# Kernel tuning notes

Hardware: AMD Instinct MI355X
Metric: run time of the kernel (lower is better)

The kernel has to match this reference:

```python
import jax, jax.numpy as jnp
import numpy as np

D_MODEL = 1024
NUM_HEAD = 16


def setup_inputs() -> dict:
    key = jax.random.key(0)
    ks = jax.random.split(key, 11)
    B, S, D = 2, 2048, D_MODEL
    scale = 1.0 / np.sqrt(D)
    inp = {
        "Q": jax.random.normal(ks[0], (B, S, D), jnp.float32),
        "K": jax.random.normal(ks[1], (B, S, D), jnp.float32),
        "V": jax.random.normal(ks[2], (B, S, D), jnp.float32),
        "Wq": jax.random.normal(ks[3], (D, D), jnp.float32) * scale,
        "bq": jax.random.normal(ks[4], (D,), jnp.float32) * 0.01,
        "Wk": jax.random.normal(ks[5], (D, D), jnp.float32) * scale,
        "bk": jax.random.normal(ks[6], (D,), jnp.float32) * 0.01,
        "Wv": jax.random.normal(ks[7], (D, D), jnp.float32) * scale,
        "bv": jax.random.normal(ks[8], (D,), jnp.float32) * 0.01,
        "Wo": jax.random.normal(ks[9], (D, D), jnp.float32) * scale,
        "bo": jax.random.normal(ks[10], (D,), jnp.float32) * 0.01,
    }
    return inp


def reference(Q, K, V, Wq, bq, Wk, bk, Wv, bv, Wo, bo):
    b, vc, d_model = Q.shape
    h = NUM_HEAD
    hd = d_model // h
    # projections (torch Linear: x @ W.T + b)
    q = (Q @ Wq.T + bq).reshape(b, vc, h, hd)
    k = (K @ Wk.T + bk).reshape(b, vc, h, hd)
    v = (V @ Wv.T + bv).reshape(b, vc, h, hd)
    # scores [b,h,q,k]
    atten = jnp.einsum('bqhd,bkhd->bhqk', q, k) / np.sqrt(hd).astype(jnp.float32)
    atten = jax.nn.softmax(atten, axis=3)
    # weighted values -> [b,q,h,hd]
    out = jnp.einsum('bhqd,bdhv->bqhv', atten, v).reshape(b, vc, d_model)
    return out @ Wo.T + bo
```

## Files before the change

### kernel.cpp

```cpp
#include <hip/hip_runtime.h>

#define S_LEN 2048
#define DM 1024
#define NH 16
#define HD 64
#define NB 2

typedef unsigned short u16;
typedef __attribute__((ext_vector_type(8))) short s16x8;
typedef __attribute__((ext_vector_type(8))) unsigned short u16x8;
typedef __attribute__((ext_vector_type(4))) float fx4;
typedef __attribute__((ext_vector_type(2))) unsigned u32x2;

__device__ __forceinline__ u16 f2bf(float f) {
  unsigned u = __builtin_bit_cast(unsigned, f);
  return (u16)((u + 0x7FFFu + ((u >> 16) & 1u)) >> 16);
}

__device__ __forceinline__ unsigned cvt_pk_bf16(float a, float b) {
  unsigned r;
  asm("v_cvt_pk_bf16_f32 %0, %1, %2" : "=v"(r) : "v"(a), "v"(b));
  return r;
}

__device__ __forceinline__ void gload16(const void* g, void* l) {
  __builtin_amdgcn_global_load_lds(
      (const __attribute__((address_space(1))) unsigned*)g,
      (__attribute__((address_space(3))) unsigned*)l, 16, 0, 0);
}

__device__ __forceinline__ fx4 mfma16(s16x8 a, s16x8 b, fx4 c) {
  return __builtin_amdgcn_mfma_f32_16x16x32_bf16(a, b, c, 0, 0, 0);
}

__global__ __launch_bounds__(256) void cvt_all_kernel(
    const float* __restrict__ Q, const float* __restrict__ K,
    const float* __restrict__ V, const float* __restrict__ Wq,
    const float* __restrict__ Wk, const float* __restrict__ Wv,
    const float* __restrict__ Wo, u16* __restrict__ Qc, u16* __restrict__ Kc,
    u16* __restrict__ Vc, u16* __restrict__ Wqb, u16* __restrict__ Wkb,
    u16* __restrict__ Wvb, u16* __restrict__ Wob) {
  const int blk = blockIdx.x;
  const float* src;
  u16* dst;
  float scale = 1.0f;
  int off;
  if (blk < 2048)      { src = Q;  dst = Qc;  off = blk; }
  else if (blk < 4096) { src = K;  dst = Kc;  off = blk - 2048; }
  else if (blk < 6144) { src = V;  dst = Vc;  off = blk - 4096; }
  else if (blk < 6656) { src = Wq; dst = Wqb; off = blk - 6144; scale = 0.18033688f; }
  else if (blk < 7168) { src = Wk; dst = Wkb; off = blk - 6656; }
  else if (blk < 7680) { src = Wv; dst = Wvb; off = blk - 7168; }
  else                 { src = Wo; dst = Wob; off = blk - 7680; }
  const int i = (off * 256 + (int)threadIdx.x) * 8;
  fx4 a = *(const fx4*)(src + i);
  fx4 b = *(const fx4*)(src + i + 4);
  u16x8 o;
  o[0] = f2bf(a[0] * scale); o[1] = f2bf(a[1] * scale);
  o[2] = f2bf(a[2] * scale); o[3] = f2bf(a[3] * scale);
  o[4] = f2bf(b[0] * scale); o[5] = f2bf(b[1] * scale);
  o[6] = f2bf(b[2] * scale); o[7] = f2bf(b[3] * scale);
  *(u16x8*)(dst + i) = o;
}

__device__ __forceinline__ void store_out(u16* C, size_t idx, float v) { C[idx] = f2bf(v); }
__device__ __forceinline__ void store_out(float* C, size_t idx, float v) { C[idx] = v; }

template <typename OUT>
__device__ __forceinline__ void gemm_pipe_body(const u16* __restrict__ A,
                                               const u16* __restrict__ Bt,
                                               const float* __restrict__ bias,
                                               float bscale, OUT* __restrict__ C,
                                               u16* __restrict__ vt, bool vout,
                                               int m0, int n0) {
  __shared__ u16 Al[3][128 * 32];
  __shared__ u16 Bl[3][128 * 32];
  const int tid = threadIdx.x;
  const int wid = tid >> 6, lane = tid & 63;
  const int g = lane >> 4, lr = lane & 15;
  const int wr = wid >> 1, wc = wid & 1;
  const int row0 = tid >> 2, ch = tid & 3;
  const int chx = ch ^ ((row0 >> 1) & 3);

  fx4 acc[4][4] = {};

  auto stage = [&](u16* Ab, u16* Bb, int k0) {
    gload16(A + (size_t)(m0 + row0) * 1024 + k0 + chx * 8, (char*)Ab + wid * 1024);
    gload16(A + (size_t)(m0 + 64 + row0) * 1024 + k0 + chx * 8,
            (char*)Ab + 4096 + wid * 1024);
    gload16(Bt + (size_t)(n0 + row0) * 1024 + k0 + chx * 8, (char*)Bb + wid * 1024);
    gload16(Bt + (size_t)(n0 + 64 + row0) * 1024 + k0 + chx * 8,
            (char*)Bb + 4096 + wid * 1024);
  };
  auto readfrag = [&](const u16* Ab, const u16* Bb, s16x8* a, s16x8* b) {
#pragma unroll
    for (int m = 0; m < 4; ++m) {
      const int row = wr * 64 + m * 16 + lr;
      a[m] = *(const s16x8*)((const char*)Ab + row * 64 + (g ^ ((row >> 1) & 3)) * 16);
    }
#pragma unroll
    for (int n = 0; n < 4; ++n) {
      const int row = wc * 64 + n * 16 + lr;
      b[n] = *(const s16x8*)((const char*)Bb + row * 64 + (g ^ ((row >> 1) & 3)) * 16);
    }
  };
  auto domfma = [&](s16x8* a, s16x8* b) {
    __builtin_amdgcn_s_setprio(1);
#pragma unroll
    for (int m = 0; m < 4; ++m)
#pragma unroll
      for (int n = 0; n < 4; ++n) acc[m][n] = mfma16(a[m], b[n], acc[m][n]);
    __builtin_amdgcn_s_setprio(0);
  };

#define GSTEP(BUF, T, NW)                                                     \
  do {                                                                        \
    asm volatile("s_waitcnt vmcnt(" #NW ")" ::: "memory");                    \
    __builtin_amdgcn_s_barrier();                                             \
    __builtin_amdgcn_sched_barrier(0);                                        \
    s16x8 afr[4], bfr[4];                                                     \
    readfrag(Al[BUF], Bl[BUF], afr, bfr);                                     \
    asm volatile("s_waitcnt lgkmcnt(0)" ::: "memory");                        \
    __builtin_amdgcn_sched_barrier(0);                                        \
    __builtin_amdgcn_s_barrier();                                             \
    __builtin_amdgcn_sched_barrier(0);                                        \
    if ((T) + 3 < 32) stage(Al[BUF], Bl[BUF], ((T) + 3) * 32);                \
    domfma(afr, bfr);                                                         \
  } while (0)

  stage(Al[0], Bl[0], 0);
  stage(Al[1], Bl[1], 32);
  stage(Al[2], Bl[2], 64);

#pragma unroll 1
  for (int t = 0; t < 30; t += 3) {
    GSTEP(0, t, 8);
    GSTEP(1, t + 1, 8);
    GSTEP(2, t + 2, 8);
  }
  GSTEP(0, 30, 4);
  GSTEP(1, 31, 0);
#undef GSTEP

  if (vout) {
#pragma unroll
    for (int n = 0; n < 4; ++n) {
      const int col = n0 + wc * 64 + n * 16 + lr;
      const float bv = bias[col] * bscale;
      const int h = col >> 6, d = col & 63;
#pragma unroll
      for (int m = 0; m < 4; ++m) {
        const int row = m0 + wr * 64 + m * 16 + g * 4;
        const int bb = row >> 11, s = row & 2047;
        u32x2 w;
        w[0] = cvt_pk_bf16(acc[m][n][0] + bv, acc[m][n][1] + bv);
        w[1] = cvt_pk_bf16(acc[m][n][2] + bv, acc[m][n][3] + bv);
        *(u32x2*)(vt + ((size_t)(((bb << 4) | h) * 64 + d)) * 2048 + s) = w;
      }
    }
  } else {
#pragma unroll
    for (int n = 0; n < 4; ++n) {
      const int col = n0 + wc * 64 + n * 16 + lr;
      const float bv = bias[col] * bscale;
#pragma unroll
      for (int m = 0; m < 4; ++m) {
        const int row = m0 + wr * 64 + m * 16 + g * 4;
#pragma unroll
        for (int j = 0; j < 4; ++j)
          store_out(C, (size_t)(row + j) * 1024 + col, acc[m][n][j] + bv);
      }
    }
  }
}

__global__ __launch_bounds__(256, 3) void gemm_qkv_kernel(
    const u16* Qc, const u16* Kc, const u16* Vc, const u16* Wq, const u16* Wk,
    const u16* Wv, const float* bq, const float* bk, const float* bv, u16* q,
    u16* k, u16* vt) {
  const int hw = blockIdx.x + (blockIdx.y << 3) + (blockIdx.z << 8);
  const int xcd = hw & 7, j = hw >> 3;
  const int x = j & 7;
  const int p = xcd + ((j >> 3) << 3);
  const int y = p & 31, z = p >> 5;

  const u16 *Ap, *Bp;
  const float* bp;
  u16* Cp;
  float bs = 1.0f;
  bool vo = false;
  if (z == 0)      { Ap = Qc; Bp = Wq; bp = bq; Cp = q; bs = 0.18033688f; }
  else if (z == 1) { Ap = Kc; Bp = Wk; bp = bk; Cp = k; }
  else             { Ap = Vc; Bp = Wv; bp = bv; Cp = q; vo = true; }
  gemm_pipe_body<u16>(Ap, Bp, bp, bs, Cp, vt, vo, y * 128, x * 128);
}

__global__ __launch_bounds__(256, 3) void gemm_out_kernel(const u16* ctx,
                                                          const u16* Wo,
                                                          const float* bo,
                                                          float* out) {
  const int hw = blockIdx.x + (blockIdx.y << 3);
  const int xcd = hw & 7, j = hw >> 3;
  const int x = j & 7;
  const int y = xcd + ((j >> 3) << 3);
  gemm_pipe_body<float>(ctx, Wo, bo, 1.0f, out, nullptr, false, y * 128, x * 128);
}

__global__ __launch_bounds__(256, 4) void attn_kernel(const u16* __restrict__ qb,
                                                      const u16* __restrict__ kb,
                                                      const u16* __restrict__ vt,
                                                      u16* __restrict__ ctx) {
  __shared__ u16 Kl[2][64 * 64];
  __shared__ u16 Vl[2][64 * 64];
  __shared__ u16 Pl[4][16 * 64];

  const int tid = threadIdx.x, wid = tid >> 6, lane = tid & 63;
  const int g = lane >> 4, lr = lane & 15;
  const int rswz = (lr & 7) * 8;
  const int pswz = (lr & 7) * 16;
  char* Pb = (char*)&Pl[wid][0];

  const int hw = blockIdx.x;
  const int xcd = hw & 7, slot = hw >> 3;
  const int bh = xcd * 4 + (slot >> 5);
  const int b = bh >> 4, h = bh & 15;
  const int q0 = (slot & 31) * 64;

  const u16* qp = qb + ((size_t)(b * S_LEN + q0 + wid * 16 + lr)) * DM + h * HD;
  s16x8 aq[2];
  aq[0] = *(const s16x8*)(qp + g * 8);
  aq[1] = *(const s16x8*)(qp + 32 + g * 8);

  fx4 accO[4] = {};
  float lrun = 0.f;

  const int srow = tid >> 3, sch = tid & 7;
  const int schx = sch ^ (srow & 7);
  const u16* kbase = kb + ((size_t)b * S_LEN) * DM + h * HD;
  const u16* vtbase = vt + ((size_t)bh * 64) * S_LEN;

#define STAGE(buf, kv)                                                             \
  do {                                                                             \
    gload16(kbase + (size_t)((kv) + srow) * DM + schx * 8,                         \
            (char*)Kl[buf] + wid * 1024);                                          \
    gload16(kbase + (size_t)((kv) + 32 + srow) * DM + schx * 8,                    \
            (char*)Kl[buf] + 4096 + wid * 1024);                                   \
    gload16(vtbase + (size_t)srow * S_LEN + (kv) + schx * 8,                       \
            (char*)Vl[buf] + wid * 1024);                                          \
    gload16(vtbase + (size_t)(32 + srow) * S_LEN + (kv) + schx * 8,                \
            (char*)Vl[buf] + 4096 + wid * 1024);                                   \
  } while (0)

  auto compute_tile = [&](const u16* Kc0, const u16* Vc0) {
    fx4 s[4] = {};
    __builtin_amdgcn_s_setprio(1);
#pragma unroll
    for (int ks = 0; ks < 2; ++ks) {
#pragma unroll
      for (int c = 0; c < 4; ++c) {
        s16x8 kf =
            *(const s16x8*)(Kc0 + (c * 16 + lr) * 64 + ((ks * 32 + g * 8) ^ rswz));
        s[c] = mfma16(kf, aq[ks], s[c]);
      }
    }
    __builtin_amdgcn_s_setprio(0);

#pragma unroll
    for (int c = 0; c < 4; ++c)
#pragma unroll
      for (int j = 0; j < 4; ++j) s[c][j] = __builtin_amdgcn_exp2f(s[c][j]);
    {
      const float r0 = (s[0][0] + s[0][1]) + (s[0][2] + s[0][3]);
      const float r1 = (s[1][0] + s[1][1]) + (s[1][2] + s[1][3]);
      const float r2 = (s[2][0] + s[2][1]) + (s[2][2] + s[2][3]);
      const float r3 = (s[3][0] + s[3][1]) + (s[3][2] + s[3][3]);
      lrun += (r0 + r1) + (r2 + r3);
    }

#pragma unroll
    for (int c = 0; c < 4; ++c) {
      u32x2 w;
      w[0] = cvt_pk_bf16(s[c][0], s[c][1]);
      w[1] = cvt_pk_bf16(s[c][2], s[c][3]);
      *(u32x2*)(Pb + lr * 128 + ((c * 32 + g * 8) ^ pswz)) = w;
    }

    __builtin_amdgcn_s_setprio(1);
#pragma unroll
    for (int ks = 0; ks < 2; ++ks) {
      s16x8 pb = *(const s16x8*)(Pb + lr * 128 + ((ks * 64 + g * 16) ^ pswz));
#pragma unroll
      for (int c = 0; c < 4; ++c) {
        s16x8 vf =
            *(const s16x8*)(Vc0 + (c * 16 + lr) * 64 + ((ks * 32 + g * 8) ^ rswz));
        accO[c] = mfma16(vf, pb, accO[c]);
      }
    }
    __builtin_amdgcn_s_setprio(0);
  };

  STAGE(0, 0);
  __syncthreads();

  for (int t = 0; t < 32; t += 2) {
    if (t + 1 < 32) STAGE(1, (t + 1) * 64);
    compute_tile(Kl[0], Vl[0]);
    __syncthreads();
    if (t + 2 < 32) STAGE(0, (t + 2) * 64);
    compute_tile(Kl[1], Vl[1]);
    __syncthreads();
  }
#undef STAGE

  lrun += __shfl_xor(lrun, 16);
  lrun += __shfl_xor(lrun, 32);
  const float inv = 1.0f / lrun;
  u16* op = ctx + ((size_t)(b * S_LEN + q0 + wid * 16 + lr)) * DM + h * HD;
#pragma unroll
  for (int c = 0; c < 4; ++c) {
    u32x2 w;
    w[0] = cvt_pk_bf16(accO[c][0] * inv, accO[c][1] * inv);
    w[1] = cvt_pk_bf16(accO[c][2] * inv, accO[c][3] * inv);
    *(u32x2*)(op + c * 16 + g * 4) = w;
  }
}

extern "C" void kernel_launch(void* const* d_in, const int* in_sizes, int n_in,
                              void* d_out, int out_size, void* d_ws, size_t ws_size,
                              hipStream_t stream) {
  const float* Q = (const float*)d_in[0];
  const float* K = (const float*)d_in[1];
  const float* V = (const float*)d_in[2];
  const float* Wq = (const float*)d_in[3];
  const float* bq = (const float*)d_in[4];
  const float* Wk = (const float*)d_in[5];
  const float* bk = (const float*)d_in[6];
  const float* Wv = (const float*)d_in[7];
  const float* bv = (const float*)d_in[8];
  const float* Wo = (const float*)d_in[9];
  const float* bo = (const float*)d_in[10];
  float* out = (float*)d_out;

  char* ws = (char*)d_ws;
  const size_t SZ_T = (size_t)NB * S_LEN * DM * 2;
  const size_t SZ_W = (size_t)DM * DM * 2;

  u16* Wqb = (u16*)(ws);
  u16* Wkb = (u16*)(ws + SZ_W);
  u16* Wvb = (u16*)(ws + 2 * SZ_W);
  u16* Wob = (u16*)(ws + 3 * SZ_W);
  u16* Qc  = (u16*)(ws + 4 * SZ_W);
  u16* Kc  = (u16*)(ws + 4 * SZ_W + SZ_T);
  u16* Vc  = (u16*)(ws + 4 * SZ_W + 2 * SZ_T);
  u16* qb  = (u16*)(ws + 4 * SZ_W + 3 * SZ_T);
  u16* kb  = (u16*)(ws + 4 * SZ_W + 4 * SZ_T);
  u16* vtb = (u16*)(ws + 4 * SZ_W + 5 * SZ_T);
  u16* ctx = Qc;

  cvt_all_kernel<<<8192, 256, 0, stream>>>(Q, K, V, Wq, Wk, Wv, Wo, Qc, Kc, Vc,
                                           Wqb, Wkb, Wvb, Wob);

  gemm_qkv_kernel<<<dim3(8, 32, 3), 256, 0, stream>>>(Qc, Kc, Vc, Wqb, Wkb, Wvb,
                                                      bq, bk, bv, qb, kb, vtb);

  attn_kernel<<<1024, 256, 0, stream>>>(qb, kb, vtb, ctx);

  gemm_out_kernel<<<dim3(8, 32), 256, 0, stream>>>(ctx, Wob, bo, out);
}
```

Before: 119.3 us.

## Switch attention to 32x32x16 MFMA with register-shuffled P, two-wave blocks

Rewrites the attention inner loop to use 32x32x16 bf16 MFMA, with each wave owning 32 query rows instead of 16. The probability tile is moved into B-operand layout through cross-half lane shuffles instead of an LDS round trip, which removes the P shared buffer. Blocks shrink to 128 threads (two waves) that still stage the same 64x64 K/V tiles, so each wave issues more loads per tile. This aims to cut LDS traffic and MFMA instruction count, at the cost of higher register pressure and fewer waves per block to hide memory latency.

```diff
diff --git a/kernel.cpp b/kernel.cpp
--- a/kernel.cpp
+++ b/kernel.cpp
@@ -10,7 +10,9 @@
 typedef __attribute__((ext_vector_type(8))) short s16x8;
 typedef __attribute__((ext_vector_type(8))) unsigned short u16x8;
 typedef __attribute__((ext_vector_type(4))) float fx4;
+typedef __attribute__((ext_vector_type(16))) float fx16;
 typedef __attribute__((ext_vector_type(2))) unsigned u32x2;
+typedef __attribute__((ext_vector_type(4))) unsigned u32x4;
 
 __device__ __forceinline__ u16 f2bf(float f) {
   unsigned u = __builtin_bit_cast(unsigned, f);
@@ -31,6 +33,10 @@
 
 __device__ __forceinline__ fx4 mfma16(s16x8 a, s16x8 b, fx4 c) {
   return __builtin_amdgcn_mfma_f32_16x16x32_bf16(a, b, c, 0, 0, 0);
+}
+
+__device__ __forceinline__ fx16 mfma32(s16x8 a, s16x8 b, fx16 c) {
+  return __builtin_amdgcn_mfma_f32_32x32x16_bf16(a, b, c, 0, 0, 0);
 }
 
 __global__ __launch_bounds__(256) void cvt_all_kernel(
@@ -206,32 +212,30 @@
   gemm_pipe_body<float>(ctx, Wo, bo, 1.0f, out, nullptr, false, y * 128, x * 128);
 }
 
-__global__ __launch_bounds__(256, 4) void attn_kernel(const u16* __restrict__ qb,
-                                                      const u16* __restrict__ kb,
-                                                      const u16* __restrict__ vt,
-                                                      u16* __restrict__ ctx) {
+__global__ __launch_bounds__(128) void attn_kernel(const u16* __restrict__ qb,
+                                                   const u16* __restrict__ kb,
+                                                   const u16* __restrict__ vt,
+                                                   u16* __restrict__ ctx) {
   __shared__ u16 Kl[2][64 * 64];
   __shared__ u16 Vl[2][64 * 64];
-  __shared__ u16 Pl[4][16 * 64];
 
   const int tid = threadIdx.x, wid = tid >> 6, lane = tid & 63;
-  const int g = lane >> 4, lr = lane & 15;
-  const int rswz = (lr & 7) * 8;
-  const int pswz = (lr & 7) * 16;
-  char* Pb = (char*)&Pl[wid][0];
+  const int q32 = lane & 31, h2 = lane >> 5, r7 = lane & 7;
+  const int rswz = r7 * 8;
 
   const int hw = blockIdx.x;
   const int xcd = hw & 7, slot = hw >> 3;
   const int bh = xcd * 4 + (slot >> 5);
   const int b = bh >> 4, h = bh & 15;
-  const int q0 = (slot & 31) * 64;
-
-  const u16* qp = qb + ((size_t)(b * S_LEN + q0 + wid * 16 + lr)) * DM + h * HD;
-  s16x8 aq[2];
-  aq[0] = *(const s16x8*)(qp + g * 8);
-  aq[1] = *(const s16x8*)(qp + 32 + g * 8);
-
-  fx4 accO[4] = {};
+  const int q0 = (slot & 31) * 64 + wid * 32;
+
+  const u16* qp = qb + ((size_t)(b * S_LEN + q0 + q32)) * DM + h * HD;
+  s16x8 aq[4];
+#pragma unroll
+  for (int kc = 0; kc < 4; ++kc)
+    aq[kc] = *(const s16x8*)(qp + kc * 16 + h2 * 8);
+
+  fx16 accO[2] = {};
   float lrun = 0.f;
 
   const int srow = tid >> 3, sch = tid & 7;
@@ -241,62 +245,61 @@
 
 #define STAGE(buf, kv)                                                             \
   do {                                                                             \
-    gload16(kbase + (size_t)((kv) + srow) * DM + schx * 8,                         \
-            (char*)Kl[buf] + wid * 1024);                                          \
-    gload16(kbase + (size_t)((kv) + 32 + srow) * DM + schx * 8,                    \
-            (char*)Kl[buf] + 4096 + wid * 1024);                                   \
-    gload16(vtbase + (size_t)srow * S_LEN + (kv) + schx * 8,                       \
-            (char*)Vl[buf] + wid * 1024);                                          \
-    gload16(vtbase + (size_t)(32 + srow) * S_LEN + (kv) + schx * 8,                \
-            (char*)Vl[buf] + 4096 + wid * 1024);                                   \
+    _Pragma("unroll") for (int p = 0; p < 4; ++p) {                                \
+      gload16(kbase + (size_t)((kv) + p * 16 + srow) * DM + schx * 8,              \
+              (char*)Kl[buf] + p * 2048 + wid * 1024);                             \
+      gload16(vtbase + (size_t)(p * 16 + srow) * S_LEN + (kv) + schx * 8,          \
+              (char*)Vl[buf] + p * 2048 + wid * 1024);                             \
+    }                                                                              \
   } while (0)
 
-  auto compute_tile = [&](const u16* Kc0, const u16* Vc0) {
-    fx4 s[4] = {};
-    __builtin_amdgcn_s_setprio(1);
-#pragma unroll
-    for (int ks = 0; ks < 2; ++ks) {
-#pragma unroll
-      for (int c = 0; c < 4; ++c) {
+  auto compute_tile = [&](const u16* Kc, const u16* Vc) {
+#pragma unroll
+    for (int sub = 0; sub < 2; ++sub) {
+      fx16 s = {};
+      __builtin_amdgcn_s_setprio(1);
+#pragma unroll
+      for (int kc = 0; kc < 4; ++kc) {
         s16x8 kf =
-            *(const s16x8*)(Kc0 + (c * 16 + lr) * 64 + ((ks * 32 + g * 8) ^ rswz));
-        s[c] = mfma16(kf, aq[ks], s[c]);
+            *(const s16x8*)(Kc + (sub * 32 + q32) * 64 + ((kc * 16 + h2 * 8) ^ rswz));
+        s = mfma32(kf, aq[kc], s);
       }
-    }
-    __builtin_amdgcn_s_setprio(0);
-
-#pragma unroll
-    for (int c = 0; c < 4; ++c)
-#pragma unroll
-      for (int j = 0; j < 4; ++j) s[c][j] = __builtin_amdgcn_exp2f(s[c][j]);
-    {
-      const float r0 = (s[0][0] + s[0][1]) + (s[0][2] + s[0][3]);
-      const float r1 = (s[1][0] + s[1][1]) + (s[1][2] + s[1][3]);
-      const float r2 = (s[2][0] + s[2][1]) + (s[2][2] + s[2][3]);
-      const float r3 = (s[3][0] + s[3][1]) + (s[3][2] + s[3][3]);
-      lrun += (r0 + r1) + (r2 + r3);
-    }
-
-#pragma unroll
-    for (int c = 0; c < 4; ++c) {
-      u32x2 w;
-      w[0] = cvt_pk_bf16(s[c][0], s[c][1]);
-      w[1] = cvt_pk_bf16(s[c][2], s[c][3]);
-      *(u32x2*)(Pb + lr * 128 + ((c * 32 + g * 8) ^ pswz)) = w;
-    }
-
-    __builtin_amdgcn_s_setprio(1);
-#pragma unroll
-    for (int ks = 0; ks < 2; ++ks) {
-      s16x8 pb = *(const s16x8*)(Pb + lr * 128 + ((ks * 64 + g * 16) ^ pswz));
-#pragma unroll
-      for (int c = 0; c < 4; ++c) {
-        s16x8 vf =
-            *(const s16x8*)(Vc0 + (c * 16 + lr) * 64 + ((ks * 32 + g * 8) ^ rswz));
-        accO[c] = mfma16(vf, pb, accO[c]);
+      __builtin_amdgcn_s_setprio(0);
+
+#pragma unroll
+      for (int j = 0; j < 16; ++j) s[j] = __builtin_amdgcn_exp2f(s[j]);
+      lrun += (((s[0] + s[1]) + (s[2] + s[3])) + ((s[4] + s[5]) + (s[6] + s[7]))) +
+              (((s[8] + s[9]) + (s[10] + s[11])) +
+               ((s[12] + s[13]) + (s[14] + s[15])));
+
+      unsigned x0 = cvt_pk_bf16(s[0], s[1]), x1 = cvt_pk_bf16(s[2], s[3]);
+      unsigned x2 = cvt_pk_bf16(s[4], s[5]), x3 = cvt_pk_bf16(s[6], s[7]);
+      unsigned x4 = cvt_pk_bf16(s[8], s[9]), x5 = cvt_pk_bf16(s[10], s[11]);
+      unsigned x6 = cvt_pk_bf16(s[12], s[13]), x7 = cvt_pk_bf16(s[14], s[15]);
+      unsigned ta = __shfl_xor(h2 ? x0 : x2, 32);
+      unsigned tb = __shfl_xor(h2 ? x1 : x3, 32);
+      unsigned tc = __shfl_xor(h2 ? x4 : x6, 32);
+      unsigned td = __shfl_xor(h2 ? x5 : x7, 32);
+      u32x4 b0, b1;
+      b0[0] = h2 ? ta : x0; b0[1] = h2 ? tb : x1;
+      b0[2] = h2 ? x2 : ta; b0[3] = h2 ? x3 : tb;
+      b1[0] = h2 ? tc : x4; b1[1] = h2 ? td : x5;
+      b1[2] = h2 ? x6 : tc; b1[3] = h2 ? x7 : td;
+      const s16x8 pb0 = __builtin_bit_cast(s16x8, b0);
+      const s16x8 pb1 = __builtin_bit_cast(s16x8, b1);
+
+      __builtin_amdgcn_s_setprio(1);
+#pragma unroll
+      for (int d0 = 0; d0 < 2; ++d0) {
+        s16x8 vf0 = *(const s16x8*)(Vc + (d0 * 32 + q32) * 64 +
+                                    ((sub * 32 + h2 * 8) ^ rswz));
+        s16x8 vf1 = *(const s16x8*)(Vc + (d0 * 32 + q32) * 64 +
+                                    ((sub * 32 + 16 + h2 * 8) ^ rswz));
+        accO[d0] = mfma32(vf0, pb0, accO[d0]);
+        accO[d0] = mfma32(vf1, pb1, accO[d0]);
       }
-    }
-    __builtin_amdgcn_s_setprio(0);
+      __builtin_amdgcn_s_setprio(0);
+    }
   };
 
   STAGE(0, 0);
@@ -312,17 +315,18 @@
   }
 #undef STAGE
 
-  lrun += __shfl_xor(lrun, 16);
   lrun += __shfl_xor(lrun, 32);
   const float inv = 1.0f / lrun;
-  u16* op = ctx + ((size_t)(b * S_LEN + q0 + wid * 16 + lr)) * DM + h * HD;
-#pragma unroll
-  for (int c = 0; c < 4; ++c) {
-    u32x2 w;
-    w[0] = cvt_pk_bf16(accO[c][0] * inv, accO[c][1] * inv);
-    w[1] = cvt_pk_bf16(accO[c][2] * inv, accO[c][3] * inv);
-    *(u32x2*)(op + c * 16 + g * 4) = w;
-  }
+  u16* op = ctx + ((size_t)(b * S_LEN + q0 + q32)) * DM + h * HD + h2 * 4;
+#pragma unroll
+  for (int d0 = 0; d0 < 2; ++d0)
+#pragma unroll
+    for (int j = 0; j < 4; ++j) {
+      u32x2 w;
+      w[0] = cvt_pk_bf16(accO[d0][4 * j] * inv, accO[d0][4 * j + 1] * inv);
+      w[1] = cvt_pk_bf16(accO[d0][4 * j + 2] * inv, accO[d0][4 * j + 3] * inv);
+      *(u32x2*)(op + d0 * 32 + 8 * j) = w;
+    }
 }
 
 extern "C" void kernel_launch(void* const* d_in, const int* in_sizes, int n_in,
@@ -363,7 +367,7 @@
   gemm_qkv_kernel<<<dim3(8, 32, 3), 256, 0, stream>>>(Qc, Kc, Vc, Wqb, Wkb, Wvb,
                                                       bq, bk, bv, qb, kb, vtb);
 
-  attn_kernel<<<1024, 256, 0, stream>>>(qb, kb, vtb, ctx);
+  attn_kernel<<<1024, 128, 0, stream>>>(qb, kb, vtb, ctx);
 
   gemm_out_kernel<<<dim3(8, 32), 256, 0, stream>>>(ctx, Wob, bo, out);
 }
```

New measurement: 126.3 us. +5.9%, slower.

## Keep softmax probabilities in registers, remap V loads to match MFMA layout

Applied to the files above, without the earlier changes.

Removes the per-wave LDS staging buffer for the bf16 probability tile. The exponentiated scores are packed straight into MFMA B-operands in registers. V fragments are now read as four 8-byte pieces per row, permuted so the k-index ordering matches the register layout of P. This cuts an LDS write/read round trip per tile and frees LDS, at the cost of narrower V reads (more LDS instructions).

```diff
diff --git a/kernel.cpp b/kernel.cpp
--- a/kernel.cpp
+++ b/kernel.cpp
@@ -11,6 +11,7 @@
 typedef __attribute__((ext_vector_type(8))) unsigned short u16x8;
 typedef __attribute__((ext_vector_type(4))) float fx4;
 typedef __attribute__((ext_vector_type(2))) unsigned u32x2;
+typedef __attribute__((ext_vector_type(4))) unsigned u32x4;
 
 __device__ __forceinline__ u16 f2bf(float f) {
   unsigned u = __builtin_bit_cast(unsigned, f);
@@ -212,13 +213,10 @@
                                                       u16* __restrict__ ctx) {
   __shared__ u16 Kl[2][64 * 64];
   __shared__ u16 Vl[2][64 * 64];
-  __shared__ u16 Pl[4][16 * 64];
 
   const int tid = threadIdx.x, wid = tid >> 6, lane = tid & 63;
   const int g = lane >> 4, lr = lane & 15;
   const int rswz = (lr & 7) * 8;
-  const int pswz = (lr & 7) * 16;
-  char* Pb = (char*)&Pl[wid][0];
 
   const int hw = blockIdx.x;
   const int xcd = hw & 7, slot = hw >> 3;
@@ -251,6 +249,12 @@
             (char*)Vl[buf] + 4096 + wid * 1024);                                   \
   } while (0)
 
+  auto vload64 = [&](const u16* Vc0, int row, int colbase) -> u32x2 {
+    const int addr =
+        row * 64 + (((colbase >> 3) ^ (row & 7)) << 3) + (colbase & 7);
+    return *(const u32x2*)(Vc0 + addr);
+  };
+
   auto compute_tile = [&](const u16* Kc0, const u16* Vc0) {
     fx4 s[4] = {};
     __builtin_amdgcn_s_setprio(1);
@@ -277,24 +281,31 @@
       lrun += (r0 + r1) + (r2 + r3);
     }
 
+    u32x4 w0, w1;
+    w0[0] = cvt_pk_bf16(s[0][0], s[0][1]);
+    w0[1] = cvt_pk_bf16(s[0][2], s[0][3]);
+    w0[2] = cvt_pk_bf16(s[1][0], s[1][1]);
+    w0[3] = cvt_pk_bf16(s[1][2], s[1][3]);
+    w1[0] = cvt_pk_bf16(s[2][0], s[2][1]);
+    w1[1] = cvt_pk_bf16(s[2][2], s[2][3]);
+    w1[2] = cvt_pk_bf16(s[3][0], s[3][1]);
+    w1[3] = cvt_pk_bf16(s[3][2], s[3][3]);
+    const s16x8 pb0 = __builtin_bit_cast(s16x8, w0);
+    const s16x8 pb1 = __builtin_bit_cast(s16x8, w1);
+
+    __builtin_amdgcn_s_setprio(1);
 #pragma unroll
     for (int c = 0; c < 4; ++c) {
-      u32x2 w;
-      w[0] = cvt_pk_bf16(s[c][0], s[c][1]);
-      w[1] = cvt_pk_bf16(s[c][2], s[c][3]);
-      *(u32x2*)(Pb + lr * 128 + ((c * 32 + g * 8) ^ pswz)) = w;
-    }
-
-    __builtin_amdgcn_s_setprio(1);
-#pragma unroll
-    for (int ks = 0; ks < 2; ++ks) {
-      s16x8 pb = *(const s16x8*)(Pb + lr * 128 + ((ks * 64 + g * 16) ^ pswz));
-#pragma unroll
-      for (int c = 0; c < 4; ++c) {
-        s16x8 vf =
-            *(const s16x8*)(Vc0 + (c * 16 + lr) * 64 + ((ks * 32 + g * 8) ^ rswz));
-        accO[c] = mfma16(vf, pb, accO[c]);
-      }
+      const int row = c * 16 + lr;
+      u32x2 a0 = vload64(Vc0, row, g * 4);
+      u32x2 a1 = vload64(Vc0, row, 16 + g * 4);
+      u32x2 a2 = vload64(Vc0, row, 32 + g * 4);
+      u32x2 a3 = vload64(Vc0, row, 48 + g * 4);
+      u32x4 m0, m1;
+      m0[0] = a0[0]; m0[1] = a0[1]; m0[2] = a1[0]; m0[3] = a1[1];
+      m1[0] = a2[0]; m1[1] = a2[1]; m1[2] = a3[0]; m1[3] = a3[1];
+      accO[c] = mfma16(__builtin_bit_cast(s16x8, m0), pb0, accO[c]);
+      accO[c] = mfma16(__builtin_bit_cast(s16x8, m1), pb1, accO[c]);
     }
     __builtin_amdgcn_s_setprio(0);
   };
```

Measured after the change: 120.7 us. Within noise of the previous version (+1.2%).

## Deepen K/V prefetch pipeline with explicit vmcnt waits and early buffer release

Applied to the files above, without the earlier changes.

Restructures the attention inner loop so two K/V tiles are in flight at once. Each step waits only for its own tile via s_waitcnt vmcnt. V fragments are read into registers right after QK, so the LDS buffer can be released and refilled with tile t+2 before the softmax and PV work runs. This is meant to hide global-load latency better and replace full __syncthreads with finer barriers. In exchange it holds V fragments in registers, raising register pressure, and relies on hand-set wait counts that must match the STAGE load count.

```diff
diff --git a/kernel.cpp b/kernel.cpp
--- a/kernel.cpp
+++ b/kernel.cpp
@@ -11,6 +11,7 @@
 typedef __attribute__((ext_vector_type(8))) unsigned short u16x8;
 typedef __attribute__((ext_vector_type(4))) float fx4;
 typedef __attribute__((ext_vector_type(2))) unsigned u32x2;
+typedef __attribute__((ext_vector_type(4))) unsigned u32x4;
 
 __device__ __forceinline__ u16 f2bf(float f) {
   unsigned u = __builtin_bit_cast(unsigned, f);
@@ -251,65 +252,74 @@
             (char*)Vl[buf] + 4096 + wid * 1024);                                   \
   } while (0)
 
-  auto compute_tile = [&](const u16* Kc0, const u16* Vc0) {
-    fx4 s[4] = {};
-    __builtin_amdgcn_s_setprio(1);
-#pragma unroll
-    for (int ks = 0; ks < 2; ++ks) {
-#pragma unroll
-      for (int c = 0; c < 4; ++c) {
-        s16x8 kf =
-            *(const s16x8*)(Kc0 + (c * 16 + lr) * 64 + ((ks * 32 + g * 8) ^ rswz));
-        s[c] = mfma16(kf, aq[ks], s[c]);
-      }
-    }
-    __builtin_amdgcn_s_setprio(0);
-
-#pragma unroll
-    for (int c = 0; c < 4; ++c)
-#pragma unroll
-      for (int j = 0; j < 4; ++j) s[c][j] = __builtin_amdgcn_exp2f(s[c][j]);
-    {
-      const float r0 = (s[0][0] + s[0][1]) + (s[0][2] + s[0][3]);
-      const float r1 = (s[1][0] + s[1][1]) + (s[1][2] + s[1][3]);
-      const float r2 = (s[2][0] + s[2][1]) + (s[2][2] + s[2][3]);
-      const float r3 = (s[3][0] + s[3][1]) + (s[3][2] + s[3][3]);
-      lrun += (r0 + r1) + (r2 + r3);
-    }
-
-#pragma unroll
-    for (int c = 0; c < 4; ++c) {
-      u32x2 w;
-      w[0] = cvt_pk_bf16(s[c][0], s[c][1]);
-      w[1] = cvt_pk_bf16(s[c][2], s[c][3]);
-      *(u32x2*)(Pb + lr * 128 + ((c * 32 + g * 8) ^ pswz)) = w;
-    }
-
-    __builtin_amdgcn_s_setprio(1);
-#pragma unroll
-    for (int ks = 0; ks < 2; ++ks) {
-      s16x8 pb = *(const s16x8*)(Pb + lr * 128 + ((ks * 64 + g * 16) ^ pswz));
-#pragma unroll
-      for (int c = 0; c < 4; ++c) {
-        s16x8 vf =
-            *(const s16x8*)(Vc0 + (c * 16 + lr) * 64 + ((ks * 32 + g * 8) ^ rswz));
-        accO[c] = mfma16(vf, pb, accO[c]);
-      }
-    }
-    __builtin_amdgcn_s_setprio(0);
-  };
+#define ASTEP(BUF, T, NW)                                                          \
+  do {                                                                             \
+    asm volatile("s_waitcnt vmcnt(" #NW ")" ::: "memory");                         \
+    __builtin_amdgcn_s_barrier();                                                  \
+    __builtin_amdgcn_sched_barrier(0);                                             \
+    fx4 s[4] = {};                                                                 \
+    s16x8 vf0[4], vf1[4];                                                          \
+    __builtin_amdgcn_s_setprio(1);                                                 \
+    _Pragma("unroll") for (int ks = 0; ks < 2; ++ks) {                             \
+      _Pragma("unroll") for (int c = 0; c < 4; ++c) {                              \
+        s16x8 kf = *(const s16x8*)(Kl[BUF] + (c * 16 + lr) * 64 +                  \
+                                   ((ks * 32 + g * 8) ^ rswz));                    \
+        s[c] = mfma16(kf, aq[ks], s[c]);                                           \
+      }                                                                            \
+    }                                                                              \
+    __builtin_amdgcn_s_setprio(0);                                                 \
+    _Pragma("unroll") for (int c = 0; c < 4; ++c) {                                \
+      vf0[c] = *(const s16x8*)(Vl[BUF] + (c * 16 + lr) * 64 + ((g * 8) ^ rswz));   \
+      vf1[c] =                                                                     \
+          *(const s16x8*)(Vl[BUF] + (c * 16 + lr) * 64 + ((32 + g * 8) ^ rswz));   \
+    }                                                                              \
+    asm volatile("s_waitcnt lgkmcnt(0)" ::: "memory");                             \
+    __builtin_amdgcn_sched_barrier(0);                                             \
+    __builtin_amdgcn_s_barrier();                                                  \
+    __builtin_amdgcn_sched_barrier(0);                                             \
+    if ((T) + 2 < 32) STAGE(BUF, ((T) + 2) * 64);                                  \
+     \
+    _Pragma("unroll") for (int c = 0; c < 4; ++c)                                  \
+        _Pragma("unroll") for (int j = 0; j < 4; ++j) s[c][j] =                    \
+        __builtin_amdgcn_exp2f(s[c][j]);                                           \
+    {                                                                              \
+      const float r0 = (s[0][0] + s[0][1]) + (s[0][2] + s[0][3]);                  \
+      const float r1 = (s[1][0] + s[1][1]) + (s[1][2] + s[1][3]);                  \
+      const float r2 = (s[2][0] + s[2][1]) + (s[2][2] + s[2][3]);                  \
+      const float r3 = (s[3][0] + s[3][1]) + (s[3][2] + s[3][3]);                  \
+      lrun += (r0 + r1) + (r2 + r3);                                               \
+    }                                                                              \
+                     \
+    _Pragma("unroll") for (int c = 0; c < 4; ++c) {                                \
+      u32x2 w;                                                                     \
+      w[0] = cvt_pk_bf16(s[c][0], s[c][1]);                                        \
+      w[1] = cvt_pk_bf16(s[c][2], s[c][3]);                                        \
+      *(u32x2*)(Pb + lr * 128 + ((c * 32 + g * 8) ^ pswz)) = w;                    \
+    }                                                                              \
+           \
+    __builtin_amdgcn_s_setprio(1);                                                 \
+    {                                                                              \
+      s16x8 pb0 = *(const s16x8*)(Pb + lr * 128 + ((g * 16) ^ pswz));              \
+      s16x8 pb1 = *(const s16x8*)(Pb + lr * 128 + ((64 + g * 16) ^ pswz));         \
+      _Pragma("unroll") for (int c = 0; c < 4; ++c) {                              \
+        accO[c] = mfma16(vf0[c], pb0, accO[c]);                                    \
+        accO[c] = mfma16(vf1[c], pb1, accO[c]);                                    \
+      }                                                                            \
+    }                                                                              \
+    __builtin_amdgcn_s_setprio(0);                                                 \
+  } while (0)
 
   STAGE(0, 0);
-  __syncthreads();
-
-  for (int t = 0; t < 32; t += 2) {
-    if (t + 1 < 32) STAGE(1, (t + 1) * 64);
-    compute_tile(Kl[0], Vl[0]);
-    __syncthreads();
-    if (t + 2 < 32) STAGE(0, (t + 2) * 64);
-    compute_tile(Kl[1], Vl[1]);
-    __syncthreads();
+  STAGE(1, 64);
+
+#pragma unroll 1
+  for (int t = 0; t < 30; t += 2) {
+    ASTEP(0, t, 4);
+    ASTEP(1, t + 1, 4);
   }
+  ASTEP(0, 30, 4);
+  ASTEP(1, 31, 0);
+#undef ASTEP
 #undef STAGE
 
   lrun += __shfl_xor(lrun, 16);
```

Measured after the change: 119.0 us. No clear change (-0.2%).
